# Kernel optimization log

Hardware: AMD Instinct MI355X
Metric: run time of the kernel (lower is better)

## Reference

```python
import jax, jax.numpy as jnp
import numpy as np

B, S, D = 2, 2048, 2048
H, HKV, HD = 32, 8, 64
G = H // HKV  # num_key_value_groups


def setup_inputs() -> dict:
    key = jax.random.key(0)
    ks = jax.random.split(key, 9)
    sc = 0.02
    return {
        "x": jax.random.normal(ks[0], (B, S, D), jnp.float32),
        "wq": jax.random.normal(ks[1], (H * HD, D), jnp.float32) * sc,
        "bq": jax.random.normal(ks[2], (H * HD,), jnp.float32) * sc,
        "wk": jax.random.normal(ks[3], (HKV * HD, D), jnp.float32) * sc,
        "bk": jax.random.normal(ks[4], (HKV * HD,), jnp.float32) * sc,
        "wv": jax.random.normal(ks[5], (HKV * HD, D), jnp.float32) * sc,
        "bv": jax.random.normal(ks[6], (HKV * HD,), jnp.float32) * sc,
        "wo": jax.random.normal(ks[7], (D, H * HD), jnp.float32) * sc,
        "bo": jax.random.normal(ks[8], (D,), jnp.float32) * sc,
    }


def reference(x, wq, bq, wk, bk, wv, bv, wo, bo):
    b, s, _ = x.shape
    # fused-QKV-style projections (nn.Linear: x @ W.T + b)
    q = (jnp.einsum("bsd,ed->bse", x, wq) + bq).reshape(b, s, H, HD)
    k = (jnp.einsum("bsd,ed->bse", x, wk) + bk).reshape(b, s, HKV, HD)
    v = (jnp.einsum("bsd,ed->bse", x, wv) + bv).reshape(b, s, HKV, HD)
    # (B, Hkv, G, S, hd): grouped query heads share a KV head — same math as
    # repeat_kv (expand+flatten) without materializing the expanded KV tensor
    q = q.transpose(0, 2, 1, 3).reshape(b, HKV, G, s, HD)
    k = k.transpose(0, 2, 1, 3)  # (B, Hkv, S, hd)
    v = v.transpose(0, 2, 1, 3)
    scale = 1.0 / jnp.sqrt(jnp.asarray(HD, x.dtype))
    scores = jnp.einsum("bkgqd,bktd->bkgqt", q, k) * scale  # (B,Hkv,G,S,S)
    causal = jnp.tril(jnp.ones((s, s), bool))
    scores = jnp.where(causal, scores, jnp.asarray(-jnp.inf, scores.dtype))
    probs = jax.nn.softmax(scores, axis=-1)
    o = jnp.einsum("bkgqt,bktd->bkgqd", probs, v)  # (B,Hkv,G,S,hd)
    o = o.reshape(b, H, s, HD).transpose(0, 2, 1, 3).reshape(b, s, H * HD)
    return jnp.einsum("bse,de->bsd", o, wo) + bo
```

## Files before the change

### kernel.cpp

```cpp
#include <hip/hip_runtime.h>
#include <hip/hip_bf16.h>
#include <cmath>

#define B_   2
#define S_   2048
#define D_   2048
#define H_   32
#define HKV_ 8
#define HD_  64

using bf16 = __hip_bfloat16;
typedef __bf16    bf16x8 __attribute__((ext_vector_type(8)));
typedef float     floatx4 __attribute__((ext_vector_type(4)));
typedef _Float16  half4 __attribute__((ext_vector_type(4)));

#if __has_builtin(__builtin_amdgcn_exp2f)
#define EXP2(x) __builtin_amdgcn_exp2f(x)
#else
#define EXP2(x) exp2f(x)
#endif

#define QSCALE 0.18033688011112042f

__device__ inline void async16(const void* g, void* l) {
  __builtin_amdgcn_global_load_lds(
      (const __attribute__((address_space(1))) void*)g,
      (__attribute__((address_space(3))) void*)l, 16, 0, 0);
}

#define MFMA32B(a, b, c) __builtin_amdgcn_mfma_f32_16x16x32_bf16((a), (b), (c), 0, 0, 0)
#define MFMA16H(a, b, c) __builtin_amdgcn_mfma_f32_16x16x16f16((a), (b), (c), 0, 0, 0)

__global__ void f2b_all(const float* __restrict__ x,  const float* __restrict__ wq,
                        const float* __restrict__ wk, const float* __restrict__ wv,
                        const float* __restrict__ wo,
                        bf16* __restrict__ xb,  bf16* __restrict__ wqb,
                        bf16* __restrict__ wkb, bf16* __restrict__ wvb,
                        bf16* __restrict__ wob) {
  const int i = blockIdx.x * blockDim.x + threadIdx.x;
  const float* src; bf16* dst; int off; float scale = 1.0f;
  if (i < 1048576)      { src = x;  dst = xb;  off = 0; }
  else if (i < 1572864) { src = wq; dst = wqb; off = 1048576; scale = QSCALE; }
  else if (i < 1703936) { src = wk; dst = wkb; off = 1572864; }
  else if (i < 1835008) { src = wv; dst = wvb; off = 1703936; }
  else                  { src = wo; dst = wob; off = 1835008; }
  const int j = i - off;
  float4 a  = ((const float4*)src)[2 * j];
  float4 b2 = ((const float4*)src)[2 * j + 1];
  alignas(16) bf16 t[8];
  t[0] = __float2bfloat16(a.x * scale);  t[1] = __float2bfloat16(a.y * scale);
  t[2] = __float2bfloat16(a.z * scale);  t[3] = __float2bfloat16(a.w * scale);
  t[4] = __float2bfloat16(b2.x * scale); t[5] = __float2bfloat16(b2.y * scale);
  t[6] = __float2bfloat16(b2.z * scale); t[7] = __float2bfloat16(b2.w * scale);
  ((uint4*)dst)[j] = *(const uint4*)t;
}

template <int MODE, typename OutT>
__device__ inline void gemm_body(const bf16* __restrict__ Ag, const bf16* __restrict__ Bg,
                                 const float* __restrict__ bias, float bscale,
                                 OutT* __restrict__ C, int Ncol, int K, int bm, int colb,
                                 bf16* As, bf16* Bs) {
  const int tid  = threadIdx.x;
  const int wid  = tid >> 6, lane = tid & 63;
  const int lm   = lane & 15, quad = lane >> 4;
  const int wm   = (wid >> 1) * 64, wn = (wid & 1) * 64;

  floatx4 acc[4][4] = {};

  const int l0 = tid * 8;
  const int r0 = l0 >> 5, c0 = l0 & 31;
  const int r1 = r0 + 64;

  for (int k0 = 0; k0 < K; k0 += 32) {
    async16(Ag + (size_t)r0 * K + k0 + c0, &As[l0]);
    async16(Ag + (size_t)r1 * K + k0 + c0, &As[l0 + 2048]);
    async16(Bg + (size_t)r0 * K + k0 + c0, &Bs[l0]);
    async16(Bg + (size_t)r1 * K + k0 + c0, &Bs[l0 + 2048]);
    asm volatile("s_waitcnt vmcnt(0)" ::: "memory");
    __syncthreads();

    bf16x8 aF[4], bF[4];
#pragma unroll
    for (int mi = 0; mi < 4; ++mi)
      aF[mi] = *(const bf16x8*)&As[(wm + mi * 16 + lm) * 32 + quad * 8];
#pragma unroll
    for (int ni = 0; ni < 4; ++ni)
      bF[ni] = *(const bf16x8*)&Bs[(wn + ni * 16 + lm) * 32 + quad * 8];
#pragma unroll
    for (int mi = 0; mi < 4; ++mi)
#pragma unroll
      for (int ni = 0; ni < 4; ++ni) {
        if constexpr (MODE == 2)
          acc[mi][ni] = MFMA32B(aF[mi], bF[ni], acc[mi][ni]);
        else
          acc[mi][ni] = MFMA32B(bF[ni], aF[mi], acc[mi][ni]);
      }
    __syncthreads();
  }

  if constexpr (MODE != 2) {
#pragma unroll
    for (int mi = 0; mi < 4; ++mi) {
      const int row = bm * 128 + wm + mi * 16 + lm;
#pragma unroll
      for (int ni = 0; ni < 4; ++ni) {
        const int col0 = colb + wn + ni * 16 + quad * 4;
        float4 bv4 = *(const float4*)&bias[col0];
        if constexpr (MODE == 0) {
          alignas(8) bf16 t4[4];
#pragma unroll
          for (int r = 0; r < 4; ++r)
            t4[r] = __float2bfloat16(acc[mi][ni][r] + ((const float*)&bv4)[r] * bscale);
          *(uint2*)&((bf16*)C)[(size_t)row * Ncol + col0] = *(const uint2*)t4;
        } else {
          float4 o4;
          o4.x = acc[mi][ni][0] + bv4.x; o4.y = acc[mi][ni][1] + bv4.y;
          o4.z = acc[mi][ni][2] + bv4.z; o4.w = acc[mi][ni][3] + bv4.w;
          *(float4*)&((float*)C)[(size_t)row * Ncol + col0] = o4;
        }
      }
    }
  } else {
#pragma unroll
    for (int mi = 0; mi < 4; ++mi) {
      const int rowg = bm * 128 + wm + mi * 16 + quad * 4;
      const int b    = rowg >> 11, s = rowg & 2047;
      const int tile = s >> 6, kvin = s & 63;
      const int kc = kvin >> 4, qd = (kvin >> 2) & 3;
#pragma unroll
      for (int ni = 0; ni < 4; ++ni) {
        const int col = colb + wn + ni * 16 + lm;
        const float bv = bias[col];
        const int kvh = col >> 6, hd = col & 63;
        const int nh = hd >> 4, lmw = hd & 15;
        const size_t base = ((size_t)((b * 8 + kvh) * 32 + tile) << 12) +
                            (((kc * 4 + nh) * 4 + qd) << 6) + (lmw << 2);
        alignas(8) _Float16 t4[4];
#pragma unroll
        for (int r = 0; r < 4; ++r)
          t4[r] = (_Float16)(acc[mi][ni][r] + bv);
        *(uint2*)&((_Float16*)C)[base] = *(const uint2*)t4;
      }
    }
  }
}

__global__ __launch_bounds__(256, 2)
void gemm_qkv(const bf16* __restrict__ xb,
              const bf16* __restrict__ wq, const bf16* __restrict__ wk,
              const bf16* __restrict__ wv,
              const float* __restrict__ bq, const float* __restrict__ bk,
              const float* __restrict__ bv,
              bf16* __restrict__ Qo, bf16* __restrict__ Ko, _Float16* __restrict__ VG) {
  __shared__ bf16 As[128 * 32];
  __shared__ bf16 Bs[128 * 32];
  const int bn = blockIdx.x, bm = blockIdx.y;
  const int K = D_;
  if (bn < 16) {
    gemm_body<0, bf16>(xb + (size_t)bm * 128 * K, wq + (size_t)(bn * 128) * K, bq, QSCALE,
                       Qo, H_ * HD_, K, bm, bn * 128, As, Bs);
  } else if (bn < 20) {
    gemm_body<0, bf16>(xb + (size_t)bm * 128 * K, wk + (size_t)((bn - 16) * 128) * K, bk, 1.0f,
                       Ko, HKV_ * HD_, K, bm, (bn - 16) * 128, As, Bs);
  } else {
    gemm_body<2, _Float16>(xb + (size_t)bm * 128 * K, wv + (size_t)((bn - 20) * 128) * K, bv, 1.0f,
                           VG, HKV_ * HD_, K, bm, (bn - 20) * 128, As, Bs);
  }
}

__global__ __launch_bounds__(256, 2)
void gemm_o(const bf16* __restrict__ A, const bf16* __restrict__ Bm,
            const float* __restrict__ bias, float* __restrict__ C,
            int Ncol, int K) {
  __shared__ bf16 As[128 * 32];
  __shared__ bf16 Bs[128 * 32];
  const int bn = blockIdx.x, bm = blockIdx.y;
  gemm_body<1, float>(A + (size_t)bm * 128 * K, Bm + (size_t)bn * 128 * K, bias, 1.0f,
                      C, Ncol, K, bm, bn * 128, As, Bs);
}

__global__ __launch_bounds__(256, 4)
void attn_kernel(const bf16* __restrict__ Q, const bf16* __restrict__ K,
                 const _Float16* __restrict__ VG, bf16* __restrict__ O) {
  const int tid = threadIdx.x;
  const int wid = tid >> 6, lane = tid & 63;
  const int lm = lane & 15, quad = lane >> 4;

  const int n   = blockIdx.y * 64 + blockIdx.x;
  const int x3  = n & 7, b1 = (n >> 3) & 1;
  const int pair = n >> 4;
  const int grp  = x3 * 2 + b1;
  const int b    = grp >> 3, kvh = grp & 7;
  const int head = kvh * 4 + wid;

  const int hi = 127 - pair, lo = pair;
  const int nt_hi = (hi >> 2) + 1;
  const int nt_lo = (lo >> 2) + 1;

  __shared__ bf16     Ks[2 * 64 * 64];
  __shared__ _Float16 Vs[2 * 64 * 64];

  const int tb[2] = {hi * 16, lo * 16};

  bf16x8 qf[2][2];
#pragma unroll
  for (int tt = 0; tt < 2; ++tt) {
    const size_t qg = ((size_t)(b * S_ + tb[tt] + lm)) * (H_ * HD_) + head * HD_;
#pragma unroll
    for (int kf = 0; kf < 2; ++kf)
      qf[tt][kf] = *(const bf16x8*)&Q[qg + kf * 32 + quad * 8];
  }

  half4 onesh;
#pragma unroll
  for (int j = 0; j < 4; ++j) onesh[j] = (_Float16)1.0f;

  floatx4 o_acc[2][4] = {};
  floatx4 lacc[2] = {};

  const int tr = tid >> 2;
  const int tc = (tid & 3) * 8;

  auto stage = [&](int t, int buf) {
#pragma unroll
    for (int c = 0; c < 2; ++c) {
      async16(&K[(size_t)(b * S_ + t * 64 + tr) * (HKV_ * HD_) + kvh * HD_ + c * 32 + tc],
              &Ks[buf * 4096 + c * 2048 + tid * 8]);
      async16(&VG[((size_t)(grp * 32 + t) << 12) + c * 2048 + tid * 8],
              &Vs[buf * 4096 + c * 2048 + tid * 8]);
    }
  };

  stage(0, 0);

  for (int t = 0; t < nt_hi; ++t) {
    const int cur = t & 1;
    asm volatile("s_waitcnt vmcnt(0)" ::: "memory");
    __syncthreads();
    if (t + 1 < nt_hi) stage(t + 1, cur ^ 1);

    const bf16*     Kb = &Ks[cur * 4096];
    const _Float16* Vb = &Vs[cur * 4096];
    const int t0 = t * 64;
    const int nact = (t < nt_lo) ? 2 : 1;

    int kcmax[2], kcross[2];
#pragma unroll
    for (int tt = 0; tt < 2; ++tt) {
      const int rel = tb[tt] + 15 - t0;
      kcmax[tt]  = (tt < nact) ? ((rel >> 4) >= 3 ? 4 : (rel >> 4) + 1) : 0;
      kcross[tt] = rel >> 4;
    }

    half4 pb[2][4];
#pragma unroll
    for (int kc = 0; kc < 4; ++kc) {
      if (kc >= kcmax[0]) break;
      bf16x8 kb0 = *(const bf16x8*)&Kb[(kc * 16 + lm) * 32 + quad * 8];
      bf16x8 kb1 = *(const bf16x8*)&Kb[2048 + (kc * 16 + lm) * 32 + quad * 8];
#pragma unroll
      for (int tt = 0; tt < 2; ++tt) {
        if (kc >= kcmax[tt]) continue;
        floatx4 sT = {};
        sT = MFMA32B(kb0, qf[tt][0], sT);
        sT = MFMA32B(kb1, qf[tt][1], sT);
        half4 pk;
        if (kc == kcross[tt]) {
          const int qrel = tb[tt] + lm - t0;
#pragma unroll
          for (int r = 0; r < 4; ++r) {
            float p = (kc * 16 + quad * 4 + r > qrel) ? 0.f : EXP2(sT[r]);
            pk[r] = (_Float16)p;
          }
        } else {
#pragma unroll
          for (int r = 0; r < 4; ++r) pk[r] = (_Float16)EXP2(sT[r]);
        }
        pb[tt][kc] = pk;
      }
    }

#pragma unroll
    for (int tt = 0; tt < 2; ++tt) {
      if (kcmax[tt] == 0) continue;
      half4 ps = pb[tt][0];
      if (kcmax[tt] > 1) ps += pb[tt][1];
      if (kcmax[tt] > 2) ps += pb[tt][2];
      if (kcmax[tt] > 3) ps += pb[tt][3];
      lacc[tt] = MFMA16H(onesh, ps, lacc[tt]);
    }

#pragma unroll
    for (int kc = 0; kc < 4; ++kc) {
      if (kc >= kcmax[0]) break;
#pragma unroll
      for (int nh = 0; nh < 4; ++nh) {
        half4 va = *(const half4*)&Vb[((kc * 4 + nh) * 4 + quad) * 64 + lm * 4];
#pragma unroll
        for (int tt = 0; tt < 2; ++tt)
          if (kc < kcmax[tt]) o_acc[tt][nh] = MFMA16H(va, pb[tt][kc], o_acc[tt][nh]);
      }
    }
  }

#pragma unroll
  for (int tt = 0; tt < 2; ++tt) {
    const float rl = 1.f / lacc[tt][0];
    const size_t rowg = (size_t)(b * S_ + tb[tt] + lm);
#pragma unroll
    for (int nh = 0; nh < 4; ++nh) {
      alignas(8) bf16 tmp[4];
#pragma unroll
      for (int r = 0; r < 4; ++r)
        tmp[r] = __float2bfloat16(o_acc[tt][nh][r] * rl);
      *(uint2*)&O[rowg * (H_ * HD_) + head * HD_ + nh * 16 + quad * 4] = *(uint2*)tmp;
    }
  }
}

extern "C" void kernel_launch(void* const* d_in, const int* in_sizes, int n_in,
                              void* d_out, int out_size, void* d_ws, size_t ws_size,
                              hipStream_t stream) {
  (void)in_sizes; (void)n_in; (void)out_size; (void)ws_size;
  const float* x  = (const float*)d_in[0];
  const float* wq = (const float*)d_in[1];
  const float* bq = (const float*)d_in[2];
  const float* wk = (const float*)d_in[3];
  const float* bk = (const float*)d_in[4];
  const float* wv = (const float*)d_in[5];
  const float* bv = (const float*)d_in[6];
  const float* wo = (const float*)d_in[7];
  const float* bo = (const float*)d_in[8];
  float* out = (float*)d_out;

  const int M = B_ * S_;
  const int E = H_ * HD_;
  const int EKV = HKV_ * HD_;

  char* ws = (char*)d_ws;
  size_t off = 0;
  auto alloc = [&](size_t bytes) {
    char* p = ws + off;
    off += (bytes + 255) & ~(size_t)255;
    return p;
  };
  bf16* xb  = (bf16*)alloc((size_t)M * D_ * 2);
  bf16* wqb = (bf16*)alloc((size_t)E * D_ * 2);
  bf16* wkb = (bf16*)alloc((size_t)EKV * D_ * 2);
  bf16* wvb = (bf16*)alloc((size_t)EKV * D_ * 2);
  bf16* wob = (bf16*)alloc((size_t)D_ * E * 2);
  bf16* Qb  = (bf16*)alloc((size_t)M * E * 2);
  bf16* Kb  = (bf16*)alloc((size_t)M * EKV * 2);
  _Float16* VG = (_Float16*)alloc((size_t)M * EKV * 2);
  bf16* Ob  = (bf16*)alloc((size_t)M * E * 2);

  f2b_all<<<9216, 256, 0, stream>>>(x, wq, wk, wv, wo, xb, wqb, wkb, wvb, wob);

  gemm_qkv<<<dim3(24, M / 128), 256, 0, stream>>>(xb, wqb, wkb, wvb, bq, bk, bv,
                                                  Qb, Kb, VG);

  attn_kernel<<<dim3(64, 16), 256, 0, stream>>>(Qb, Kb, VG, Ob);

  gemm_o<<<dim3(D_ / 128, M / 128), 256, 0, stream>>>(Ob, wob, bo, out, D_, D_);
}
```

Before: 295.3 us.

## Double-buffer GEMM LDS tiles and pack attention probabilities with cvt_pkrtz

The shared GEMM body now double-buffers its LDS tiles. Loads for the next K-slice are issued right after the barrier, so they overlap the MFMAs on the current slice, and one barrier per iteration is removed. Launch bounds for both GEMMs rise from 2 to 3 blocks per SM to keep occupancy despite the doubled LDS. Separately, the attention kernel converts exp2 outputs to fp16 in pairs with the packed round-toward-zero conversion, which changes the rounding mode slightly.

```diff
diff --git a/kernel.cpp b/kernel.cpp
--- a/kernel.cpp
+++ b/kernel.cpp
@@ -13,6 +13,7 @@
 typedef __bf16    bf16x8 __attribute__((ext_vector_type(8)));
 typedef float     floatx4 __attribute__((ext_vector_type(4)));
 typedef _Float16  half4 __attribute__((ext_vector_type(4)));
+typedef __fp16    fp16x2 __attribute__((ext_vector_type(2)));
 
 #if __has_builtin(__builtin_amdgcn_exp2f)
 #define EXP2(x) __builtin_amdgcn_exp2f(x)
@@ -26,6 +27,13 @@
   __builtin_amdgcn_global_load_lds(
       (const __attribute__((address_space(1))) void*)g,
       (__attribute__((address_space(3))) void*)l, 16, 0, 0);
+}
+
+__device__ inline half4 pack4(float a, float b, float c, float d) {
+  union { fp16x2 h2[2]; half4 h4; } u;
+  u.h2[0] = __builtin_amdgcn_cvt_pkrtz(a, b);
+  u.h2[1] = __builtin_amdgcn_cvt_pkrtz(c, d);
+  return u.h4;
 }
 
 #define MFMA32B(a, b, c) __builtin_amdgcn_mfma_f32_16x16x32_bf16((a), (b), (c), 0, 0, 0)
@@ -71,21 +79,31 @@
   const int r0 = l0 >> 5, c0 = l0 & 31;
   const int r1 = r0 + 64;
 
+  auto stage = [&](int k0, int buf) {
+    const int o = buf * 4096;
+    async16(Ag + (size_t)r0 * K + k0 + c0, &As[o + l0]);
+    async16(Ag + (size_t)r1 * K + k0 + c0, &As[o + l0 + 2048]);
+    async16(Bg + (size_t)r0 * K + k0 + c0, &Bs[o + l0]);
+    async16(Bg + (size_t)r1 * K + k0 + c0, &Bs[o + l0 + 2048]);
+  };
+
+  stage(0, 0);
+
   for (int k0 = 0; k0 < K; k0 += 32) {
-    async16(Ag + (size_t)r0 * K + k0 + c0, &As[l0]);
-    async16(Ag + (size_t)r1 * K + k0 + c0, &As[l0 + 2048]);
-    async16(Bg + (size_t)r0 * K + k0 + c0, &Bs[l0]);
-    async16(Bg + (size_t)r1 * K + k0 + c0, &Bs[l0 + 2048]);
+    const int cur = (k0 >> 5) & 1;
     asm volatile("s_waitcnt vmcnt(0)" ::: "memory");
     __syncthreads();
-
+    if (k0 + 32 < K) stage(k0 + 32, cur ^ 1);
+
+    const bf16* Ab = &As[cur * 4096];
+    const bf16* Bb = &Bs[cur * 4096];
     bf16x8 aF[4], bF[4];
 #pragma unroll
     for (int mi = 0; mi < 4; ++mi)
-      aF[mi] = *(const bf16x8*)&As[(wm + mi * 16 + lm) * 32 + quad * 8];
+      aF[mi] = *(const bf16x8*)&Ab[(wm + mi * 16 + lm) * 32 + quad * 8];
 #pragma unroll
     for (int ni = 0; ni < 4; ++ni)
-      bF[ni] = *(const bf16x8*)&Bs[(wn + ni * 16 + lm) * 32 + quad * 8];
+      bF[ni] = *(const bf16x8*)&Bb[(wn + ni * 16 + lm) * 32 + quad * 8];
 #pragma unroll
     for (int mi = 0; mi < 4; ++mi)
 #pragma unroll
@@ -95,7 +113,6 @@
         else
           acc[mi][ni] = MFMA32B(bF[ni], aF[mi], acc[mi][ni]);
       }
-    __syncthreads();
   }
 
   if constexpr (MODE != 2) {
@@ -145,15 +162,15 @@
   }
 }
 
-__global__ __launch_bounds__(256, 2)
+__global__ __launch_bounds__(256, 3)
 void gemm_qkv(const bf16* __restrict__ xb,
               const bf16* __restrict__ wq, const bf16* __restrict__ wk,
               const bf16* __restrict__ wv,
               const float* __restrict__ bq, const float* __restrict__ bk,
               const float* __restrict__ bv,
               bf16* __restrict__ Qo, bf16* __restrict__ Ko, _Float16* __restrict__ VG) {
-  __shared__ bf16 As[128 * 32];
-  __shared__ bf16 Bs[128 * 32];
+  __shared__ bf16 As[2 * 128 * 32];
+  __shared__ bf16 Bs[2 * 128 * 32];
   const int bn = blockIdx.x, bm = blockIdx.y;
   const int K = D_;
   if (bn < 16) {
@@ -168,12 +185,12 @@
   }
 }
 
-__global__ __launch_bounds__(256, 2)
+__global__ __launch_bounds__(256, 3)
 void gemm_o(const bf16* __restrict__ A, const bf16* __restrict__ Bm,
             const float* __restrict__ bias, float* __restrict__ C,
             int Ncol, int K) {
-  __shared__ bf16 As[128 * 32];
-  __shared__ bf16 Bs[128 * 32];
+  __shared__ bf16 As[2 * 128 * 32];
+  __shared__ bf16 Bs[2 * 128 * 32];
   const int bn = blockIdx.x, bm = blockIdx.y;
   gemm_body<1, float>(A + (size_t)bm * 128 * K, Bm + (size_t)bn * 128 * K, bias, 1.0f,
                       C, Ncol, K, bm, bn * 128, As, Bs);
@@ -264,19 +281,17 @@
         floatx4 sT = {};
         sT = MFMA32B(kb0, qf[tt][0], sT);
         sT = MFMA32B(kb1, qf[tt][1], sT);
-        half4 pk;
+        float p[4];
         if (kc == kcross[tt]) {
           const int qrel = tb[tt] + lm - t0;
 #pragma unroll
-          for (int r = 0; r < 4; ++r) {
-            float p = (kc * 16 + quad * 4 + r > qrel) ? 0.f : EXP2(sT[r]);
-            pk[r] = (_Float16)p;
-          }
+          for (int r = 0; r < 4; ++r)
+            p[r] = (kc * 16 + quad * 4 + r > qrel) ? 0.f : EXP2(sT[r]);
         } else {
 #pragma unroll
-          for (int r = 0; r < 4; ++r) pk[r] = (_Float16)EXP2(sT[r]);
+          for (int r = 0; r < 4; ++r) p[r] = EXP2(sT[r]);
         }
-        pb[tt][kc] = pk;
+        pb[tt][kc] = pack4(p[0], p[1], p[2], p[3]);
       }
     }
 
```

Measured after the change: 297.9 us. No clear change (+0.9%).
